# Kernel optimization log

Measured on AMD Instinct MI355X. Metric: run time of the kernel, lower is better.

Reference implementation:

```python
import jax, jax.numpy as jnp
import numpy as np


def setup_inputs() -> dict:
    key = jax.random.key(0)
    k1, k2, k3 = jax.random.split(key, 3)
    B, D, L = 16384, 1024, 4
    x = jax.random.normal(k1, (B, D), dtype=jnp.float32)
    weights = jax.random.normal(k2, (L, D, 1), dtype=jnp.float32)
    biases = jax.random.normal(k3, (L, D, 1), dtype=jnp.float32)
    return {"x": x, "weights": weights, "biases": biases}


def reference(x, weights, biases):
    # DCN cross layer. Literal torch math per layer:
    #   out = (x[:,:,None] @ out[:,None,:] @ w_i + b_i).squeeze(-1) + out
    # Algebraically identical (associativity of matmul):
    #   out = x * (out @ w_i) + b_i.T + out
    w = weights[..., 0]  # (L, D)
    b = biases[..., 0]   # (L, D)

    def step(out, wb):
        w_i, b_i = wb
        s = out @ w_i  # (B,) scalar per row: out . w_i
        out = x * s[:, None] + b_i[None, :] + out
        return out, None

    out, _ = jax.lax.scan(step, x, (w, b))
    return out
```

## Files before the change

kernel.cpp:

```cpp
#include <hip/hip_runtime.h>


constexpr int D = 1024;
constexpr int L = 4;
constexpr int WAVES_PER_BLOCK = 4;

__global__ __launch_bounds__(256) void cross_layer_kernel(
    const float* __restrict__ x,
    const float* __restrict__ w,
    const float* __restrict__ b,
    float* __restrict__ out,
    int B)
{
    const int lane = threadIdx.x & 63;
    const int wave = threadIdx.x >> 6;
    const int row  = blockIdx.x * WAVES_PER_BLOCK + wave;
    if (row >= B) return;

    const float4* x4 = reinterpret_cast<const float4*>(x + (size_t)row * D);

    float4 xr[4], o[4];
    #pragma unroll
    for (int c = 0; c < 4; ++c) {
        xr[c] = x4[lane + c * 64];
        o[c]  = xr[c];
    }

    #pragma unroll
    for (int l = 0; l < L; ++l) {
        const float4* w4 = reinterpret_cast<const float4*>(w + (size_t)l * D);
        const float4* b4 = reinterpret_cast<const float4*>(b + (size_t)l * D);

        float4 wr[4];
        #pragma unroll
        for (int c = 0; c < 4; ++c) wr[c] = w4[lane + c * 64];

        float partial = 0.f;
        #pragma unroll
        for (int c = 0; c < 4; ++c) {
            partial += o[c].x * wr[c].x + o[c].y * wr[c].y
                     + o[c].z * wr[c].z + o[c].w * wr[c].w;
        }
        #pragma unroll
        for (int off = 32; off >= 1; off >>= 1)
            partial += __shfl_xor(partial, off, 64);
        const float s = partial;

        #pragma unroll
        for (int c = 0; c < 4; ++c) {
            float4 br = b4[lane + c * 64];
            o[c].x = fmaf(xr[c].x, s, br.x + o[c].x);
            o[c].y = fmaf(xr[c].y, s, br.y + o[c].y);
            o[c].z = fmaf(xr[c].z, s, br.z + o[c].z);
            o[c].w = fmaf(xr[c].w, s, br.w + o[c].w);
        }
    }

    float4* out4 = reinterpret_cast<float4*>(out + (size_t)row * D);
    #pragma unroll
    for (int c = 0; c < 4; ++c) out4[lane + c * 64] = o[c];
}

extern "C" void kernel_launch(void* const* d_in, const int* in_sizes, int n_in,
                              void* d_out, int out_size, void* d_ws, size_t ws_size,
                              hipStream_t stream) {
    const float* x  = (const float*)d_in[0];
    const float* w  = (const float*)d_in[1];
    const float* b  = (const float*)d_in[2];
    float* out      = (float*)d_out;

    const int B = in_sizes[0] / D;
    const int blocks = (B + WAVES_PER_BLOCK - 1) / WAVES_PER_BLOCK;
    cross_layer_kernel<<<blocks, 256, 0, stream>>>(x, w, b, out, B);
}
```

Baseline: 124.3 us.

## Collapse cross layers into one affine form with precomputed bias prefix sums

The kernel rewrites the layer recurrence so each output row is x*A + cumulative bias. A depends only on four dot products of x with the weights plus bias-weight constants computed once per block. It also stages weights and bias prefix sums in shared memory, has each wave handle four rows to amortise that setup, and uses nontemporal loads and stores. The goal is to remove the serial per-layer reductions and the repeated weight and bias loads. The cost is a per-block setup pass, a block barrier, and reassociated floating-point arithmetic.

```diff
diff --git a/kernel.cpp b/kernel.cpp
--- a/kernel.cpp
+++ b/kernel.cpp
@@ -1,9 +1,14 @@
 #include <hip/hip_runtime.h>
 
 
-constexpr int D = 1024;
-constexpr int L = 4;
+typedef float v4f __attribute__((ext_vector_type(4)));
+
+constexpr int D  = 1024;
+constexpr int D4 = D / 4;
+constexpr int L  = 4;
 constexpr int WAVES_PER_BLOCK = 4;
+constexpr int ROWS_PER_WAVE   = 4;
+constexpr int ROWS_PER_BLOCK  = WAVES_PER_BLOCK * ROWS_PER_WAVE;
 
 __global__ __launch_bounds__(256) void cross_layer_kernel(
     const float* __restrict__ x,
@@ -12,53 +17,100 @@
     float* __restrict__ out,
     int B)
 {
-    const int lane = threadIdx.x & 63;
-    const int wave = threadIdx.x >> 6;
-    const int row  = blockIdx.x * WAVES_PER_BLOCK + wave;
-    if (row >= B) return;
+    __shared__ v4f sw [L * D4];
+    __shared__ v4f spb[L * D4];
 
-    const float4* x4 = reinterpret_cast<const float4*>(x + (size_t)row * D);
+    const int tid = threadIdx.x;
 
-    float4 xr[4], o[4];
+    const v4f* w4 = reinterpret_cast<const v4f*>(w);
+    const v4f* b4 = reinterpret_cast<const v4f*>(b);
     #pragma unroll
-    for (int c = 0; c < 4; ++c) {
-        xr[c] = x4[lane + c * 64];
-        o[c]  = xr[c];
+    for (int l = 0; l < L; ++l)
+        sw[l * D4 + tid] = w4[l * D4 + tid];
+    {
+        v4f p = (v4f)(0.f);
+        #pragma unroll
+        for (int l = 0; l < L; ++l) {
+            p += b4[l * D4 + tid];
+            spb[l * D4 + tid] = p;
+        }
+    }
+    __syncthreads();
+
+    const int lane = tid & 63;
+    const int wave = tid >> 6;
+
+    v4f wr[L][4];
+    #pragma unroll
+    for (int l = 0; l < L; ++l)
+        #pragma unroll
+        for (int c = 0; c < 4; ++c)
+            wr[l][c] = sw[l * D4 + lane + c * 64];
+
+    v4f csum[4];
+    #pragma unroll
+    for (int c = 0; c < 4; ++c)
+        csum[c] = spb[(L - 1) * D4 + lane + c * 64];
+
+    float e[3];
+    #pragma unroll
+    for (int l = 1; l < L; ++l) {
+        float part = 0.f;
+        #pragma unroll
+        for (int c = 0; c < 4; ++c) {
+            v4f pb = spb[(l - 1) * D4 + lane + c * 64];
+            v4f pr = pb * wr[l][c];
+            part += pr.x + pr.y + pr.z + pr.w;
+        }
+        e[l - 1] = part;
+    }
+    #pragma unroll
+    for (int off = 32; off >= 1; off >>= 1) {
+        #pragma unroll
+        for (int k = 0; k < 3; ++k)
+            e[k] += __shfl_xor(e[k], off, 64);
     }
 
+    const int row0 = blockIdx.x * ROWS_PER_BLOCK + wave * ROWS_PER_WAVE;
     #pragma unroll
-    for (int l = 0; l < L; ++l) {
-        const float4* w4 = reinterpret_cast<const float4*>(w + (size_t)l * D);
-        const float4* b4 = reinterpret_cast<const float4*>(b + (size_t)l * D);
+    for (int r = 0; r < ROWS_PER_WAVE; ++r) {
+        const int row = row0 + r;
+        if (row >= B) break;
 
-        float4 wr[4];
+        const v4f* x4 = reinterpret_cast<const v4f*>(x + (size_t)row * D);
+        v4f xr[4];
         #pragma unroll
-        for (int c = 0; c < 4; ++c) wr[c] = w4[lane + c * 64];
+        for (int c = 0; c < 4; ++c)
+            xr[c] = __builtin_nontemporal_load(&x4[lane + c * 64]);
 
-        float partial = 0.f;
+        float dd[4];
+        #pragma unroll
+        for (int l = 0; l < L; ++l) {
+            v4f acc = xr[0] * wr[l][0];
+            #pragma unroll
+            for (int c = 1; c < 4; ++c)
+                acc += xr[c] * wr[l][c];
+            dd[l] = acc.x + acc.y + acc.z + acc.w;
+        }
+        #pragma unroll
+        for (int off = 32; off >= 1; off >>= 1) {
+            #pragma unroll
+            for (int k = 0; k < 4; ++k)
+                dd[k] += __shfl_xor(dd[k], off, 64);
+        }
+
+        float A = 1.f + dd[0];
+        A = A + A * dd[1] + e[0];
+        A = A + A * dd[2] + e[1];
+        A = A + A * dd[3] + e[2];
+
+        v4f* o4 = reinterpret_cast<v4f*>(out + (size_t)row * D);
         #pragma unroll
         for (int c = 0; c < 4; ++c) {
-            partial += o[c].x * wr[c].x + o[c].y * wr[c].y
-                     + o[c].z * wr[c].z + o[c].w * wr[c].w;
-        }
-        #pragma unroll
-        for (int off = 32; off >= 1; off >>= 1)
-            partial += __shfl_xor(partial, off, 64);
-        const float s = partial;
-
-        #pragma unroll
-        for (int c = 0; c < 4; ++c) {
-            float4 br = b4[lane + c * 64];
-            o[c].x = fmaf(xr[c].x, s, br.x + o[c].x);
-            o[c].y = fmaf(xr[c].y, s, br.y + o[c].y);
-            o[c].z = fmaf(xr[c].z, s, br.z + o[c].z);
-            o[c].w = fmaf(xr[c].w, s, br.w + o[c].w);
+            v4f v = xr[c] * A + csum[c];
+            __builtin_nontemporal_store(v, &o4[lane + c * 64]);
         }
     }
-
-    float4* out4 = reinterpret_cast<float4*>(out + (size_t)row * D);
-    #pragma unroll
-    for (int c = 0; c < 4; ++c) out4[lane + c * 64] = o[c];
 }
 
 extern "C" void kernel_launch(void* const* d_in, const int* in_sizes, int n_in,
@@ -70,6 +122,6 @@
     float* out      = (float*)d_out;
 
     const int B = in_sizes[0] / D;
-    const int blocks = (B + WAVES_PER_BLOCK - 1) / WAVES_PER_BLOCK;
+    const int blocks = (B + ROWS_PER_BLOCK - 1) / ROWS_PER_BLOCK;
     cross_layer_kernel<<<blocks, 256, 0, stream>>>(x, w, b, out, B);
 }
```

After: 122.8 us. No clear change (-1.2%).
